# Kernel optimization log

Measured on AMD Instinct MI355X. Metric: run time of the kernel, lower is better.

The kernel has to match this reference:

```python
import jax, jax.numpy as jnp
import numpy as np


def setup_inputs() -> dict:
    key = jax.random.key(0)
    k = jax.random.split(key, 5)
    B, N, F = 1024, 256, 6
    H, O = 128, 64
    return {
        "x": jax.random.normal(k[0], (B, N, F), dtype=jnp.float32),
        "W1": jax.random.normal(k[1], (F, H), dtype=jnp.float32) * 0.2,
        "b1": jax.random.normal(k[2], (H,), dtype=jnp.float32) * 0.1,
        "W2": jax.random.normal(k[3], (H, O), dtype=jnp.float32) * 0.1,
        "b2": jax.random.normal(k[4], (O,), dtype=jnp.float32) * 0.1,
    }


def _gcn_norm_adj(x, valid):
    """Dense, vectorized version of the per-batch edge loop + GCN normalization.

    Edge (i,j), i!=j, exists among valid nodes iff cond_i or cond_j, where
    cond = (feat[3] != 0) or (feat[4] != 0). GCNConv adds self-loops on the
    valid subgraph and applies symmetric D^{-1/2} (A+I) D^{-1/2} normalization.
    """
    B, N, _ = x.shape
    cond = (x[..., 3] != 0) | (x[..., 4] != 0)              # [B, N]
    pair = cond[:, :, None] | cond[:, None, :]              # [B, N, N]
    vv = valid[:, :, None] & valid[:, None, :]
    not_diag = ~jnp.eye(N, dtype=bool)[None]
    off = (pair & vv & not_diag).astype(x.dtype)            # off-diagonal edges
    self_loops = jnp.eye(N, dtype=x.dtype)[None] * valid[:, :, None].astype(x.dtype)
    A = off + self_loops                                    # [B, N, N]
    deg = A.sum(-1)                                         # [B, N]
    dinv = jnp.where(deg > 0, jax.lax.rsqrt(jnp.maximum(deg, 1.0)) * (deg > 0), 0.0)
    dinv = jnp.where(deg > 0, deg ** -0.5, 0.0)
    return dinv[:, :, None] * A * dinv[:, None, :]          # [B, N, N]


def reference(x, W1, b1, W2, b2):
    # valid node mask: any nonzero feature
    valid = jnp.abs(x).sum(-1) != 0                         # [B, N]
    An = _gcn_norm_adj(x, valid)

    # GCNConv 1: aggregate(norm_adj, x @ W1) + b1, then ReLU
    h = jax.nn.relu(jnp.einsum("bij,bjh->bih", An, x @ W1) + b1)
    # GCNConv 2
    h = jnp.einsum("bij,bjo->bio", An, h @ W2) + b2         # [B, N, O]

    # global mean pool over valid nodes only (invalid rows excluded)
    vm = valid.astype(h.dtype)
    summed = jnp.einsum("bno,bn->bo", h, vm)
    cnt = vm.sum(-1, keepdims=True)                         # [B, 1]
    return jnp.where(cnt > 0, summed / jnp.maximum(cnt, 1.0), 0.0)
```

## Files before the change

kernel.cpp:

```cpp
#include <hip/hip_runtime.h>
#include <math.h>


#define NB 1024
#define NN 256
#define NF 6
#define NH 128
#define NO 64

template <int CTRL, int ROW_MASK, int BANK_MASK>
__device__ __forceinline__ float dpp_add(float v) {
    int moved = __builtin_amdgcn_update_dpp(0, __float_as_int(v),
                                            CTRL, ROW_MASK, BANK_MASK, true);
    return v + __int_as_float(moved);
}

__device__ __forceinline__ float wave_sum64(float v) {
    v = dpp_add<0x111, 0xf, 0xf>(v);
    v = dpp_add<0x112, 0xf, 0xf>(v);
    v = dpp_add<0x114, 0xf, 0xe>(v);
    v = dpp_add<0x118, 0xf, 0xc>(v);
    v = dpp_add<0x142, 0xa, 0xf>(v);
    v = dpp_add<0x143, 0xc, 0xf>(v);
    return v;
}

__device__ __forceinline__ float bcast63(float v) {
    return __int_as_float(__builtin_amdgcn_readlane(__float_as_int(v), 63));
}

__global__ __launch_bounds__(64) void gnn_kernel(
    const float* __restrict__ x,
    const float* __restrict__ W1,
    const float* __restrict__ b1,
    const float* __restrict__ W2,
    const float* __restrict__ b2,
    float* __restrict__ out)
{
    const int b    = blockIdx.x;
    const int lane = threadIdx.x;

    __shared__ float hC_s[NH];
    __shared__ float hN_s[NH];

    float w1a[NF], w1b[NF];
    #pragma unroll
    for (int f = 0; f < NF; ++f) {
        w1a[f] = W1[f * NH + lane];
        w1b[f] = W1[f * NH + lane + 64];
    }
    const float b1a = b1[lane];
    const float b1b = b1[lane + 64];
    const float b2r = b2[lane];

    const float* xb = x + (size_t)b * NN * NF;
    float xf[4][NF];
    bool  ncf[4];
    float r[15];
    #pragma unroll
    for (int j = 0; j < 15; ++j) r[j] = 0.f;

    #pragma unroll
    for (int k = 0; k < 4; ++k) {
        const float2* p = (const float2*)(xb + (size_t)(lane + 64 * k) * NF);
        float2 u0 = p[0], u1 = p[1], u2 = p[2];
        xf[k][0] = u0.x; xf[k][1] = u0.y; xf[k][2] = u1.x;
        xf[k][3] = u1.y; xf[k][4] = u2.x; xf[k][5] = u2.y;

        float absum = fabsf(xf[k][0]) + fabsf(xf[k][1]) + fabsf(xf[k][2])
                    + fabsf(xf[k][3]) + fabsf(xf[k][4]) + fabsf(xf[k][5]);
        const bool valid = (absum != 0.f);
        const bool condv = valid && ((xf[k][3] != 0.f) || (xf[k][4] != 0.f));
        const bool isNC  = valid && !condv;
        ncf[k] = isNC;

        if (valid) r[12] += 1.f;
        if (condv) {
            r[13] += 1.f;
            #pragma unroll
            for (int f = 0; f < NF; ++f) r[f] += xf[k][f];
        } else if (isNC) {
            r[14] += 1.f;
            #pragma unroll
            for (int f = 0; f < NF; ++f) r[f + 6] += xf[k][f];
        }
    }

    #pragma unroll
    for (int j = 0; j < 15; ++j) r[j] = wave_sum64(r[j]);

    float fs[12];
    #pragma unroll
    for (int j = 0; j < 12; ++j) fs[j] = bcast63(r[j]);
    const int nv  = (int)bcast63(r[12]);
    const int nc  = (int)bcast63(r[13]);
    const int nnc = (int)bcast63(r[14]);

    if (nv == 0) {
        out[(size_t)b * NO + lane] = 0.f;
        return;
    }

    const float a  = 1.f / sqrtf((float)nv);
    const float c  = 1.f / sqrtf((float)(nc + 1));
    const float c2 = c * c;

    float zc0 = 0.f, zn0 = 0.f, zc1 = 0.f, zn1 = 0.f;
    #pragma unroll
    for (int f = 0; f < NF; ++f) {
        zc0 = fmaf(fs[f],     w1a[f], zc0);
        zn0 = fmaf(fs[f + 6], w1a[f], zn0);
        zc1 = fmaf(fs[f],     w1b[f], zc1);
        zn1 = fmaf(fs[f + 6], w1b[f], zn1);
    }
    const float Sc0   = a * zc0,            Sc1   = a * zc1;
    const float Sall0 = Sc0 + c * zn0,      Sall1 = Sc1 + c * zn1;

    const float hCa = fmaxf(fmaf(a, Sall0, b1a), 0.f);
    const float hCb = fmaxf(fmaf(a, Sall1, b1b), 0.f);

    float acc0 = 0.f, acc1 = 0.f;
    if (nnc > 0) {
        const float vl0 = fmaf(c, Sc0, b1a);
        const float vl1 = fmaf(c, Sc1, b1b);
        #pragma unroll
        for (int k = 0; k < 4; ++k) {
            unsigned long long m = __ballot(ncf[k]);
            while (m) {
                const int l = (int)__ffsll((long long)m) - 1;
                m &= m - 1;
                float sf[NF];
                #pragma unroll
                for (int f = 0; f < NF; ++f)
                    sf[f] = __int_as_float(
                        __builtin_amdgcn_readlane(__float_as_int(xf[k][f]), l));
                float z0 = 0.f, z1 = 0.f;
                #pragma unroll
                for (int f = 0; f < NF; ++f) {
                    z0 = fmaf(sf[f], w1a[f], z0);
                    z1 = fmaf(sf[f], w1b[f], z1);
                }
                acc0 += fmaxf(fmaf(c2, z0, vl0), 0.f);
                acc1 += fmaxf(fmaf(c2, z1, vl1), 0.f);
            }
        }
    }

    hC_s[lane]      = hCa;
    hC_s[lane + 64] = hCb;
    hN_s[lane]      = acc0;
    hN_s[lane + 64] = acc1;
    __syncthreads();

    const float4* hv = (const float4*)hC_s;
    const float4* nv4 = (const float4*)hN_s;
    float y2C = 0.f, y2N = 0.f;
    #pragma unroll
    for (int h4 = 0; h4 < NH / 4; ++h4) {
        const float4 sC = hv[h4];
        const float4 sN = nv4[h4];
        const int hh = h4 * 4;
        const float w0 = W2[(hh + 0) * NO + lane];
        const float w1 = W2[(hh + 1) * NO + lane];
        const float w2 = W2[(hh + 2) * NO + lane];
        const float w3 = W2[(hh + 3) * NO + lane];
        y2C = fmaf(sC.x, w0, y2C);  y2N = fmaf(sN.x, w0, y2N);
        y2C = fmaf(sC.y, w1, y2C);  y2N = fmaf(sN.y, w1, y2N);
        y2C = fmaf(sC.z, w2, y2C);  y2N = fmaf(sN.z, w2, y2N);
        y2C = fmaf(sC.w, w3, y2C);  y2N = fmaf(sN.w, w3, y2N);
    }

    const float S2c   = a * (float)nc * y2C;
    const float S2all = S2c + c * y2N;
    const float pooled = (float)nc * (a * S2all)
                       + (float)(nv - nc) * (c * S2c)
                       + c2 * y2N
                       + (float)nv * b2r;
    out[(size_t)b * NO + lane] = pooled / (float)nv;
}

extern "C" void kernel_launch(void* const* d_in, const int* in_sizes, int n_in,
                              void* d_out, int out_size, void* d_ws, size_t ws_size,
                              hipStream_t stream) {
    const float* x  = (const float*)d_in[0];
    const float* W1 = (const float*)d_in[1];
    const float* b1 = (const float*)d_in[2];
    const float* W2 = (const float*)d_in[3];
    const float* b2 = (const float*)d_in[4];
    float* out = (float*)d_out;

    gnn_kernel<<<NB, 64, 0, stream>>>(x, W1, b1, W2, b2, out);
}
```

Before: 9.938 us.

## Fold pooling coefficients before W2 GEMV, use ballot counts and contiguous loads

Counts of valid, conditioned and non-conditioned nodes now come from ballot+popcount rather than three extra wave reductions. Each lane loads its 4 nodes as six contiguous float4s, which reassigns nodes to lanes. The second layer folds the pooling coefficients into a single combined hidden vector before the W2 product. That product is done with readlane broadcasts instead of shared memory and a barrier, halving the FMAs and dropping LDS traffic. The trade-off is 128 scalar readlanes and float rounding that differs slightly from before.

```diff
diff --git a/kernel.cpp b/kernel.cpp
--- a/kernel.cpp
+++ b/kernel.cpp
@@ -29,6 +29,10 @@
     return __int_as_float(__builtin_amdgcn_readlane(__float_as_int(v), 63));
 }
 
+__device__ __forceinline__ float rdlane(float v, int l) {
+    return __int_as_float(__builtin_amdgcn_readlane(__float_as_int(v), l));
+}
+
 __global__ __launch_bounds__(64) void gnn_kernel(
     const float* __restrict__ x,
     const float* __restrict__ W1,
@@ -40,9 +44,6 @@
     const int b    = blockIdx.x;
     const int lane = threadIdx.x;
 
-    __shared__ float hC_s[NH];
-    __shared__ float hN_s[NH];
-
     float w1a[NF], w1b[NF];
     #pragma unroll
     for (int f = 0; f < NF; ++f) {
@@ -53,20 +54,24 @@
     const float b1b = b1[lane + 64];
     const float b2r = b2[lane];
 
-    const float* xb = x + (size_t)b * NN * NF;
-    float xf[4][NF];
-    bool  ncf[4];
-    float r[15];
+    const float4* xp = (const float4*)(x + (size_t)b * NN * NF
+                                         + (size_t)lane * 4 * NF);
+    float4 q0 = xp[0], q1 = xp[1], q2 = xp[2], q3 = xp[3], q4 = xp[4], q5 = xp[5];
+    float xf[4][NF] = {
+        { q0.x, q0.y, q0.z, q0.w, q1.x, q1.y },
+        { q1.z, q1.w, q2.x, q2.y, q2.z, q2.w },
+        { q3.x, q3.y, q3.z, q3.w, q4.x, q4.y },
+        { q4.z, q4.w, q5.x, q5.y, q5.z, q5.w },
+    };
+
+    bool ncf[4];
+    float r[12];
     #pragma unroll
-    for (int j = 0; j < 15; ++j) r[j] = 0.f;
+    for (int j = 0; j < 12; ++j) r[j] = 0.f;
+    int nv = 0, nc = 0, nnc = 0;
 
     #pragma unroll
     for (int k = 0; k < 4; ++k) {
-        const float2* p = (const float2*)(xb + (size_t)(lane + 64 * k) * NF);
-        float2 u0 = p[0], u1 = p[1], u2 = p[2];
-        xf[k][0] = u0.x; xf[k][1] = u0.y; xf[k][2] = u1.x;
-        xf[k][3] = u1.y; xf[k][4] = u2.x; xf[k][5] = u2.y;
-
         float absum = fabsf(xf[k][0]) + fabsf(xf[k][1]) + fabsf(xf[k][2])
                     + fabsf(xf[k][3]) + fabsf(xf[k][4]) + fabsf(xf[k][5]);
         const bool valid = (absum != 0.f);
@@ -74,27 +79,24 @@
         const bool isNC  = valid && !condv;
         ncf[k] = isNC;
 
-        if (valid) r[12] += 1.f;
+        nv  += (int)__popcll(__ballot(valid));
+        nc  += (int)__popcll(__ballot(condv));
+        nnc += (int)__popcll(__ballot(isNC));
+
         if (condv) {
-            r[13] += 1.f;
             #pragma unroll
             for (int f = 0; f < NF; ++f) r[f] += xf[k][f];
         } else if (isNC) {
-            r[14] += 1.f;
             #pragma unroll
             for (int f = 0; f < NF; ++f) r[f + 6] += xf[k][f];
         }
     }
 
     #pragma unroll
-    for (int j = 0; j < 15; ++j) r[j] = wave_sum64(r[j]);
-
+    for (int j = 0; j < 12; ++j) r[j] = wave_sum64(r[j]);
     float fs[12];
     #pragma unroll
     for (int j = 0; j < 12; ++j) fs[j] = bcast63(r[j]);
-    const int nv  = (int)bcast63(r[12]);
-    const int nc  = (int)bcast63(r[13]);
-    const int nnc = (int)bcast63(r[14]);
 
     if (nv == 0) {
         out[(size_t)b * NO + lane] = 0.f;
@@ -113,8 +115,8 @@
         zc1 = fmaf(fs[f],     w1b[f], zc1);
         zn1 = fmaf(fs[f + 6], w1b[f], zn1);
     }
-    const float Sc0   = a * zc0,            Sc1   = a * zc1;
-    const float Sall0 = Sc0 + c * zn0,      Sall1 = Sc1 + c * zn1;
+    const float Sc0   = a * zc0,       Sc1   = a * zc1;
+    const float Sall0 = Sc0 + c * zn0, Sall1 = Sc1 + c * zn1;
 
     const float hCa = fmaxf(fmaf(a, Sall0, b1a), 0.f);
     const float hCb = fmaxf(fmaf(a, Sall1, b1b), 0.f);
@@ -131,9 +133,7 @@
                 m &= m - 1;
                 float sf[NF];
                 #pragma unroll
-                for (int f = 0; f < NF; ++f)
-                    sf[f] = __int_as_float(
-                        __builtin_amdgcn_readlane(__float_as_int(xf[k][f]), l));
+                for (int f = 0; f < NF; ++f) sf[f] = rdlane(xf[k][f], l);
                 float z0 = 0.f, z1 = 0.f;
                 #pragma unroll
                 for (int f = 0; f < NF; ++f) {
@@ -146,37 +146,20 @@
         }
     }
 
-    hC_s[lane]      = hCa;
-    hC_s[lane + 64] = hCb;
-    hN_s[lane]      = acc0;
-    hN_s[lane + 64] = acc1;
-    __syncthreads();
+    const float alpha = a * (float)nc * ((float)nc * a + (float)(nv - nc) * c);
+    const float beta  = c * ((float)nc * a + c);
+    const float inv_nv = 1.f / (float)nv;
+    const float ga = (alpha * hCa + beta * acc0) * inv_nv;
+    const float gb = (alpha * hCb + beta * acc1) * inv_nv;
 
-    const float4* hv = (const float4*)hC_s;
-    const float4* nv4 = (const float4*)hN_s;
-    float y2C = 0.f, y2N = 0.f;
+    float y = 0.f;
     #pragma unroll
-    for (int h4 = 0; h4 < NH / 4; ++h4) {
-        const float4 sC = hv[h4];
-        const float4 sN = nv4[h4];
-        const int hh = h4 * 4;
-        const float w0 = W2[(hh + 0) * NO + lane];
-        const float w1 = W2[(hh + 1) * NO + lane];
-        const float w2 = W2[(hh + 2) * NO + lane];
-        const float w3 = W2[(hh + 3) * NO + lane];
-        y2C = fmaf(sC.x, w0, y2C);  y2N = fmaf(sN.x, w0, y2N);
-        y2C = fmaf(sC.y, w1, y2C);  y2N = fmaf(sN.y, w1, y2N);
-        y2C = fmaf(sC.z, w2, y2C);  y2N = fmaf(sN.z, w2, y2N);
-        y2C = fmaf(sC.w, w3, y2C);  y2N = fmaf(sN.w, w3, y2N);
+    for (int hh = 0; hh < 64; ++hh) {
+        y = fmaf(rdlane(ga, hh), W2[hh * NO + lane],        y);
+        y = fmaf(rdlane(gb, hh), W2[(hh + 64) * NO + lane], y);
     }
 
-    const float S2c   = a * (float)nc * y2C;
-    const float S2all = S2c + c * y2N;
-    const float pooled = (float)nc * (a * S2all)
-                       + (float)(nv - nc) * (c * S2c)
-                       + c2 * y2N
-                       + (float)nv * b2r;
-    out[(size_t)b * NO + lane] = pooled / (float)nv;
+    out[(size_t)b * NO + lane] = y + b2r;
 }
 
 extern "C" void kernel_launch(void* const* d_in, const int* in_sizes, int n_in,
```

Result: slower. 10.22 us (+2.8%).
